# Kernel tuning notes

Hardware: AMD Instinct MI355X
Metric: run time of the kernel (lower is better)

## Reference

```python
import jax, jax.numpy as jnp
import numpy as np


def setup_inputs() -> dict:
    key = jax.random.key(0)
    x = jax.random.normal(key, (256, 1024), dtype=jnp.float32)
    return {"x": x}


def reference(x):
    # SelMul: for input row [a, b, c] output is [a*a, a*b, a*c, b*b, b*c, c*c],
    # i.e. x[:, i] * x[:, j] for all i <= j, in row-major upper-triangular order.
    # The torch original materializes the full n^2 outer product then slices;
    # here we gather only the n(n+1)/2 needed pairs directly.
    n = x.shape[-1]
    rows, cols = jnp.triu_indices(n)  # rows[k] <= cols[k], row-major order
    return x[:, rows] * x[:, cols]  # (B, n*(n+1)//2)
```

## Files before the change

### kernel.cpp

```cpp
#include <hip/hip_runtime.h>


#define N 1024
#define TRI (N * (N + 1) / 2)
#define TRI4 (TRI / 4)
#define TPB 256
#define NBLOCKS 8192

__global__ __launch_bounds__(TPB) void selmul_kernel(const float* __restrict__ x,
                                                     float* __restrict__ out,
                                                     int total4) {
    const int stride = gridDim.x * TPB;
    for (int v = blockIdx.x * TPB + threadIdx.x; v < total4; v += stride) {
        const int b = (int)((unsigned)v / TRI4);
        const int r = (v - b * TRI4) << 2;

        const float s = sqrtf(4198401.0f - 8.0f * (float)r);
        int i = (int)((2049.0f - s) * 0.5f);
        int rs = (i * (2049 - i)) >> 1;
        if (rs > r) {
            --i;
            rs = (i * (2049 - i)) >> 1;
        } else {
            const int rs1 = ((i + 1) * (2048 - i)) >> 1;
            if (rs1 <= r) { ++i; rs = rs1; }
        }
        int j = i + (r - rs);

        const float* __restrict__ xrow = x + b * N;
        float xi = xrow[i];
        float4 o;
        o.x = xi * xrow[j];
        if (++j >= N) { ++i; j = i; xi = xrow[i]; }
        o.y = xi * xrow[j];
        if (++j >= N) { ++i; j = i; xi = xrow[i]; }
        o.z = xi * xrow[j];
        if (++j >= N) { ++i; j = i; xi = xrow[i]; }
        o.w = xi * xrow[j];

        ((float4*)out)[v] = o;
    }
}

extern "C" void kernel_launch(void* const* d_in, const int* in_sizes, int n_in,
                              void* d_out, int out_size, void* d_ws, size_t ws_size,
                              hipStream_t stream) {
    const float* x = (const float*)d_in[0];
    float* out = (float*)d_out;
    const int total4 = out_size >> 2;
    selmul_kernel<<<NBLOCKS, TPB, 0, stream>>>(x, out, total4);
}
```

Before: 603.2 us.

## Stage input row in LDS and write triangle rows with paired balancing

Replaces the per-float4 sqrt-based index inversion with a row-oriented scheme. Each block loads one batch row into shared memory and writes whole triangular output rows, pairing row i with row N-1-i so every block gets equal work. Rows are written with an unaligned head, a float4 body and a scalar tail. This removes the per-element index math and the repeated global gathers. In exchange, short rows leave most threads idle, and loop overhead and sync costs are added.

```diff
diff --git a/kernel.cpp b/kernel.cpp
--- a/kernel.cpp
+++ b/kernel.cpp
@@ -3,42 +3,60 @@
 
 #define N 1024
 #define TRI (N * (N + 1) / 2)
-#define TRI4 (TRI / 4)
 #define TPB 256
-#define NBLOCKS 8192
+#define PAIRS 64
+#define CHUNKS (N / 2 / PAIRS)
+#define NBLOCKS (256 * CHUNKS)
+
+__device__ __forceinline__ void row_copy(float* __restrict__ outb,
+                                         const float* __restrict__ sx,
+                                         int i, int t) {
+    const int L = N - i;
+    const int rs = (i * (2 * N + 1 - i)) >> 1;
+    const float xi = sx[i];
+    float* const dst = outb + rs;
+
+    int h = (4 - (rs & 3)) & 3;
+    h = (h < L) ? h : L;
+    if (t < h) dst[t] = xi * sx[i + t];
+
+    const int nb4 = (L - h) >> 2;
+    for (int m = t; m < nb4; m += TPB) {
+        const int k = h + (m << 2);
+        const float* __restrict__ s = sx + i + k;
+        float4 v;
+        v.x = xi * s[0];
+        v.y = xi * s[1];
+        v.z = xi * s[2];
+        v.w = xi * s[3];
+        *reinterpret_cast<float4*>(dst + k) = v;
+    }
+
+    const int tail = (L - h) & 3;
+    if (t < tail) {
+        const int k = h + (nb4 << 2) + t;
+        dst[k] = xi * sx[i + k];
+    }
+}
 
 __global__ __launch_bounds__(TPB) void selmul_kernel(const float* __restrict__ x,
-                                                     float* __restrict__ out,
-                                                     int total4) {
-    const int stride = gridDim.x * TPB;
-    for (int v = blockIdx.x * TPB + threadIdx.x; v < total4; v += stride) {
-        const int b = (int)((unsigned)v / TRI4);
-        const int r = (v - b * TRI4) << 2;
+                                                     float* __restrict__ out) {
+    __shared__ float sx[N];
+    const int b = blockIdx.x / CHUNKS;
+    const int c = blockIdx.x % CHUNKS;
+    const int t = threadIdx.x;
 
-        const float s = sqrtf(4198401.0f - 8.0f * (float)r);
-        int i = (int)((2049.0f - s) * 0.5f);
-        int rs = (i * (2049 - i)) >> 1;
-        if (rs > r) {
-            --i;
-            rs = (i * (2049 - i)) >> 1;
-        } else {
-            const int rs1 = ((i + 1) * (2048 - i)) >> 1;
-            if (rs1 <= r) { ++i; rs = rs1; }
-        }
-        int j = i + (r - rs);
+    reinterpret_cast<float4*>(sx)[t] =
+        reinterpret_cast<const float4*>(x + b * N)[t];
+    __syncthreads();
 
-        const float* __restrict__ xrow = x + b * N;
-        float xi = xrow[i];
-        float4 o;
-        o.x = xi * xrow[j];
-        if (++j >= N) { ++i; j = i; xi = xrow[i]; }
-        o.y = xi * xrow[j];
-        if (++j >= N) { ++i; j = i; xi = xrow[i]; }
-        o.z = xi * xrow[j];
-        if (++j >= N) { ++i; j = i; xi = xrow[i]; }
-        o.w = xi * xrow[j];
-
-        ((float4*)out)[v] = o;
+    float* const outb = out + (size_t)b * TRI;
+    const int i0 = c * PAIRS;
+#pragma unroll 1
+    for (int p = 0; p < PAIRS; ++p) {
+        const int i = i0 + p;
+        row_copy(outb, sx, i, t);
+        row_copy(outb, sx, (N - 1) - i, t);
     }
 }
 
@@ -47,6 +65,5 @@
                               hipStream_t stream) {
     const float* x = (const float*)d_in[0];
     float* out = (float*)d_out;
-    const int total4 = out_size >> 2;
-    selmul_kernel<<<NBLOCKS, TPB, 0, stream>>>(x, out, total4);
+    selmul_kernel<<<NBLOCKS, TPB, 0, stream>>>(x, out);
 }
```

New measurement: 608.1 us. About the same (+0.8%).
